# Performance work log

Measured on AMD Instinct MI355X. Metric: run time of the kernel, lower is better.

Reference implementation:

```python
import jax, jax.numpy as jnp
import numpy as np

V_THRESH = 0.3

@jax.custom_vjp
def spike(x):
    return (x > 0).astype(x.dtype)

def _spike_fwd(x):
    return spike(x), x

def _spike_bwd(x, g):
    # rectangular straight-through surrogate gradient (pass grad where |x| < 0.5)
    return (g * (jnp.abs(x) < 0.5).astype(g.dtype),)

spike.defvjp(_spike_fwd, _spike_bwd)


def setup_inputs() -> dict:
    key = jax.random.key(0)
    B, T, H = 128, 2048, 128
    k1, = jax.random.split(key, 1)
    x_seq = jax.random.normal(k1, (B, T, H), dtype=jnp.float32)
    v0 = jnp.zeros((B, H), dtype=jnp.float32)
    z0 = jnp.zeros((B, H), dtype=jnp.float32)
    decay_raw = jnp.zeros((H,), dtype=jnp.float32)  # nn.initializers.constant(0.0)
    return {"x_seq": x_seq, "v0": v0, "z0": z0, "decay_raw": decay_raw}


def reference(x_seq, v0, z0, decay_raw):
    # LIF recurrence: v_t = v_{t-1} * decay * (1 - z_{t-1}) + x_t ; z_t = spike(v_t - v_thresh)
    decay = jax.nn.sigmoid(decay_raw)  # (H,)

    def step(carry, x_t):
        v, z = carry
        v = v * decay * (1.0 - z) + x_t
        z_out = spike(v - V_THRESH)
        return (v, z_out), z_out

    x_tb = jnp.swapaxes(x_seq, 0, 1)  # [T, B, H] for lax.scan over time
    (_, _), spk_tb = jax.lax.scan(step, (v0, z0), x_tb)
    return jnp.swapaxes(spk_tb, 0, 1)  # [B, T, H]
```

## Files before the change

### kernel.cpp

```cpp
#include <hip/hip_runtime.h>
#include <math.h>


constexpr int Bdim  = 128;
constexpr int Tdim  = 2048;
constexpr int Hdim  = 128;
constexpr int HW    = 64;
constexpr int CHUNK = 256;
constexpr int WARM  = 96;
constexpr int NCH   = Tdim / CHUNK;
constexpr float VTH = 0.3f;

__global__ __launch_bounds__(64) void lif_kernel(
    const float* __restrict__ x,
    const float* __restrict__ v0,
    const float* __restrict__ z0,
    const float* __restrict__ decay_raw,
    float* __restrict__ out)
{
    const int lane = threadIdx.x;
    const int blk  = blockIdx.x;
    const int c    = blk & (NCH - 1);
    const int g    = blk >> 3;
    const int b    = g >> 1;
    const int h    = (g & 1) * HW + lane;

    const float d  = 1.0f / (1.0f + expf(-decay_raw[h]));
    const int t0     = c * CHUNK;
    const int tstart = (c == 0) ? 0 : (t0 - WARM);
    const int nwb    = (c == 0) ? 0 : (WARM / 8);
    const int nbatch = nwb + CHUNK / 8;

    float v; bool zb;
    if (c == 0) { v = v0[b * Hdim + h]; zb = z0[b * Hdim + h] > 0.5f; }
    else        { v = 0.0f;             zb = false; }

    const float* xl = x   + ((size_t)b * Tdim + tstart) * Hdim + h;
    float*       ol = out + ((size_t)b * Tdim + tstart) * Hdim + h;

    float xq[4][8];
    #pragma unroll
    for (int q = 0; q < 3; ++q)
        #pragma unroll
        for (int j = 0; j < 8; ++j)
            xq[q][j] = xl[(size_t)(q * 8 + j) * Hdim];

#define LIF_BATCH(FB, P, STORE)                                               \
    {                                                                         \
        const int fb_ = (FB);                                                 \
        if (fb_ + 3 < nbatch) {                                               \
            _Pragma("unroll")                                                 \
            for (int j = 0; j < 8; ++j)                                       \
                xq[((P) + 3) & 3][j] = xl[(size_t)((fb_ + 3) * 8 + j) * Hdim];\
        }                                                                     \
        float zv[8];                                                          \
        _Pragma("unroll")                                                     \
        for (int j = 0; j < 8; ++j) {                                         \
            const float xv = xq[(P)][j];                                      \
            const float vd = v * d;                                           \
            v  = (zb ? 0.0f : vd) + xv;         \
            zb = v > VTH;                                                     \
            zv[j] = zb ? 1.0f : 0.0f;                                         \
        }                                                                     \
        if (STORE) {                                                          \
            _Pragma("unroll")                                                 \
            for (int j = 0; j < 8; ++j)                                       \
                ol[(size_t)(fb_ * 8 + j) * Hdim] = zv[j];                     \
        }                                                                     \
    }

    for (int ob = 0; ob < nwb / 4; ++ob) {
        LIF_BATCH(ob * 4 + 0, 0, false)
        LIF_BATCH(ob * 4 + 1, 1, false)
        LIF_BATCH(ob * 4 + 2, 2, false)
        LIF_BATCH(ob * 4 + 3, 3, false)
    }
    for (int ob = 0; ob < CHUNK / 32; ++ob) {
        const int base = nwb + ob * 4;
        LIF_BATCH(base + 0, 0, true)
        LIF_BATCH(base + 1, 1, true)
        LIF_BATCH(base + 2, 2, true)
        LIF_BATCH(base + 3, 3, true)
    }
#undef LIF_BATCH
}

extern "C" void kernel_launch(void* const* d_in, const int* in_sizes, int n_in,
                              void* d_out, int out_size, void* d_ws, size_t ws_size,
                              hipStream_t stream) {
    const float* x         = (const float*)d_in[0];
    const float* v0        = (const float*)d_in[1];
    const float* z0        = (const float*)d_in[2];
    const float* decay_raw = (const float*)d_in[3];
    float* out = (float*)d_out;

    lif_kernel<<<(Bdim * Hdim / HW) * NCH, 64, 0, stream>>>(x, v0, z0, decay_raw, out);
}
```

Measured before the change: 252.8 us.

## Shorten warmup, deepen prefetch, and defer spike stores via bit-packed LDS

Cuts the warmup window from 96 to 64 steps, which relies on the spike reset forgetting old state quickly enough to still give exact results. The prefetch ring grows from 4 to 8 batches so more loads are in flight. Spikes are packed into bitmasks and kept in shared memory, then all stores happen after the recurrence, taking memory writes off the serial dependency chain. The shorter warmup risks mismatches if the state has not converged by the chunk start, and the extra registers may reduce occupancy.

```diff
diff --git a/kernel.cpp b/kernel.cpp
--- a/kernel.cpp
+++ b/kernel.cpp
@@ -7,9 +7,11 @@
 constexpr int Hdim  = 128;
 constexpr int HW    = 64;
 constexpr int CHUNK = 256;
-constexpr int WARM  = 96;
+constexpr int WARM  = 64;
 constexpr int NCH   = Tdim / CHUNK;
 constexpr float VTH = 0.3f;
+
+static_assert(WARM % 8 == 0 && CHUNK % 64 == 0, "phase alignment");
 
 __global__ __launch_bounds__(64) void lif_kernel(
     const float* __restrict__ x,
@@ -18,6 +20,8 @@
     const float* __restrict__ decay_raw,
     float* __restrict__ out)
 {
+    __shared__ unsigned zw[4][2][64];
+
     const int lane = threadIdx.x;
     const int blk  = blockIdx.x;
     const int c    = blk & (NCH - 1);
@@ -25,64 +29,97 @@
     const int b    = g >> 1;
     const int h    = (g & 1) * HW + lane;
 
-    const float d  = 1.0f / (1.0f + expf(-decay_raw[h]));
-    const int t0     = c * CHUNK;
-    const int tstart = (c == 0) ? 0 : (t0 - WARM);
-    const int nwb    = (c == 0) ? 0 : (WARM / 8);
-    const int nbatch = nwb + CHUNK / 8;
+    const float d = 1.0f / (1.0f + expf(-decay_raw[h]));
 
     float v; bool zb;
     if (c == 0) { v = v0[b * Hdim + h]; zb = z0[b * Hdim + h] > 0.5f; }
     else        { v = 0.0f;             zb = false; }
 
+    const int t0     = c * CHUNK;
+    const int tstart = (c == 0) ? 0 : (t0 - WARM);
     const float* xl = x   + ((size_t)b * Tdim + tstart) * Hdim + h;
-    float*       ol = out + ((size_t)b * Tdim + tstart) * Hdim + h;
+    float*       ol = out + ((size_t)b * Tdim + t0)     * Hdim + h;
 
-    float xq[4][8];
+    float xq[8][8];
+
+#define PREF(SLOT, TGT)                                                 \
+    { _Pragma("unroll")                                                 \
+      for (int j_ = 0; j_ < 8; ++j_)                                    \
+          xq[SLOT][j_] = xl[(size_t)((TGT) * 8 + j_) * Hdim]; }
+#define STEPW(XV) \
+    { const float vd_ = v * d; v = (zb ? 0.0f : vd_) + (XV); zb = v > VTH; }
+#define STEPR(XV, W, BIT)                                               \
+    { const float vd_ = v * d; v = (zb ? 0.0f : vd_) + (XV);            \
+      zb = v > VTH; W |= (zb ? (BIT) : 0u); }
+
     #pragma unroll
-    for (int q = 0; q < 3; ++q)
+    for (int q = 0; q < 7; ++q)
+        PREF(q, q)
+
+    if (c != 0) {
         #pragma unroll
-        for (int j = 0; j < 8; ++j)
-            xq[q][j] = xl[(size_t)(q * 8 + j) * Hdim];
-
-#define LIF_BATCH(FB, P, STORE)                                               \
-    {                                                                         \
-        const int fb_ = (FB);                                                 \
-        if (fb_ + 3 < nbatch) {                                               \
-            _Pragma("unroll")                                                 \
-            for (int j = 0; j < 8; ++j)                                       \
-                xq[((P) + 3) & 3][j] = xl[(size_t)((fb_ + 3) * 8 + j) * Hdim];\
-        }                                                                     \
-        float zv[8];                                                          \
-        _Pragma("unroll")                                                     \
-        for (int j = 0; j < 8; ++j) {                                         \
-            const float xv = xq[(P)][j];                                      \
-            const float vd = v * d;                                           \
-            v  = (zb ? 0.0f : vd) + xv;         \
-            zb = v > VTH;                                                     \
-            zv[j] = zb ? 1.0f : 0.0f;                                         \
-        }                                                                     \
-        if (STORE) {                                                          \
-            _Pragma("unroll")                                                 \
-            for (int j = 0; j < 8; ++j)                                       \
-                ol[(size_t)(fb_ * 8 + j) * Hdim] = zv[j];                     \
-        }                                                                     \
+        for (int q = 0; q < 8; ++q) {
+            PREF((q + 7) & 7, q + 7)
+            #pragma unroll
+            for (int j = 0; j < 8; ++j) STEPW(xq[q][j])
+        }
+        xl += (size_t)WARM * Hdim;
     }
 
-    for (int ob = 0; ob < nwb / 4; ++ob) {
-        LIF_BATCH(ob * 4 + 0, 0, false)
-        LIF_BATCH(ob * 4 + 1, 1, false)
-        LIF_BATCH(ob * 4 + 2, 2, false)
-        LIF_BATCH(ob * 4 + 3, 3, false)
+    #pragma unroll 1
+    for (int ob = 0; ob < 3; ++ob) {
+        unsigned w0 = 0, w1 = 0;
+        const int rb = ob * 8;
+        #pragma unroll
+        for (int q = 0; q < 8; ++q) {
+            PREF((q + 7) & 7, rb + q + 7)
+            if (q < 4) {
+                #pragma unroll
+                for (int j = 0; j < 8; ++j)
+                    STEPR(xq[q][j], w0, 1u << ((q & 3) * 8 + j))
+            } else {
+                #pragma unroll
+                for (int j = 0; j < 8; ++j)
+                    STEPR(xq[q][j], w1, 1u << ((q & 3) * 8 + j))
+            }
+        }
+        zw[ob][0][lane] = w0;
+        zw[ob][1][lane] = w1;
     }
-    for (int ob = 0; ob < CHUNK / 32; ++ob) {
-        const int base = nwb + ob * 4;
-        LIF_BATCH(base + 0, 0, true)
-        LIF_BATCH(base + 1, 1, true)
-        LIF_BATCH(base + 2, 2, true)
-        LIF_BATCH(base + 3, 3, true)
+    {
+        unsigned w0 = 0, w1 = 0;
+        PREF(7, 31)
+        #pragma unroll
+        for (int j = 0; j < 8; ++j) STEPR(xq[0][j], w0, 1u << j)
+        #pragma unroll
+        for (int q = 1; q < 4; ++q)
+            #pragma unroll
+            for (int j = 0; j < 8; ++j)
+                STEPR(xq[q][j], w0, 1u << (q * 8 + j))
+        #pragma unroll
+        for (int q = 4; q < 8; ++q)
+            #pragma unroll
+            for (int j = 0; j < 8; ++j)
+                STEPR(xq[q][j], w1, 1u << ((q - 4) * 8 + j))
+        zw[3][0][lane] = w0;
+        zw[3][1][lane] = w1;
     }
-#undef LIF_BATCH
+
+    #pragma unroll 1
+    for (int ob = 0; ob < 4; ++ob) {
+        const unsigned w0 = zw[ob][0][lane];
+        const unsigned w1 = zw[ob][1][lane];
+        float* o = ol + (size_t)(ob * 64) * Hdim;
+        #pragma unroll
+        for (int t = 0; t < 32; ++t)
+            o[(size_t)t * Hdim] = ((w0 >> t) & 1u) ? 1.0f : 0.0f;
+        #pragma unroll
+        for (int t = 0; t < 32; ++t)
+            o[(size_t)(32 + t) * Hdim] = ((w1 >> t) & 1u) ? 1.0f : 0.0f;
+    }
+#undef PREF
+#undef STEPW
+#undef STEPR
 }
 
 extern "C" void kernel_launch(void* const* d_in, const int* in_sizes, int n_in,
```

Result: no change. 251.3 us (-0.6%).
